# Performance work log

Hardware: AMD Instinct MI355X
Metric: run time of the kernel (lower is better)

The kernel has to match this reference:

```python
import jax, jax.numpy as jnp
import numpy as np

B, C1, C2, H, W = 16, 64, 64, 160, 160
K, KS, HID = 4, 3, 16  # K kernels, 3x3, hidden = max(int(64/16),16)=16
EPS = 1e-5


def setup_inputs() -> dict:
    key = jax.random.key(0)
    ks = jax.random.split(key, 8)
    fan_out = KS * KS * C2
    return {
        "x": jax.random.normal(ks[0], (B, C1, H, W), jnp.float32),
        # K candidate conv kernels and biases
        "Wk": jax.random.normal(ks[1], (K, C2, C1, KS, KS), jnp.float32) * np.sqrt(2.0 / fan_out),
        "bk": jnp.zeros((K, C2), jnp.float32),
        # attention trunk: 1x1 conv C1->HID (no bias), BN, ReLU
        "Wfc": jax.random.normal(ks[2], (HID, C1), jnp.float32) * 0.1,
        "gamma_h": jnp.ones((HID,), jnp.float32),
        "beta_h": jnp.zeros((HID,), jnp.float32),
        # four attention heads
        "Wf": jax.random.normal(ks[3], (C2, HID), jnp.float32) * 0.1,
        "bf": jnp.zeros((C2,), jnp.float32),
        "Ws": jax.random.normal(ks[4], (KS * KS, HID), jnp.float32) * 0.1,
        "bs": jnp.zeros((KS * KS,), jnp.float32),
        "Wc": jax.random.normal(ks[5], (C1, HID), jnp.float32) * 0.1,
        "bc": jnp.zeros((C1,), jnp.float32),
        "Ww": jax.random.normal(ks[6], (K, HID), jnp.float32) * 0.1,
        "bw": jnp.zeros((K,), jnp.float32),
        # outer BatchNorm2d params
        "gamma_o": jnp.ones((C2,), jnp.float32),
        "beta_o": jnp.zeros((C2,), jnp.float32),
    }


def reference(x, Wk, bk, Wfc, gamma_h, beta_h, Wf, bf, Ws, bs, Wc, bc, Ww, bw, gamma_o, beta_o):
    # ---- per-sample attention over K kernels ----
    ctx = x.mean(axis=(2, 3))                      # (B, C1)  global avg pool
    h = ctx @ Wfc.T                                # (B, HID) 1x1 conv == linear
    mu = h.mean(axis=0)
    var = h.var(axis=0)                            # biased, as torch BN training
    h = (h - mu) / jnp.sqrt(var + EPS) * gamma_h + beta_h
    h = jax.nn.relu(h)
    attn_f = jax.nn.sigmoid(h @ Wf.T + bf)         # (B, C2)
    attn_s = jax.nn.sigmoid(h @ Ws.T + bs).reshape(B, KS, KS)
    attn_c = jax.nn.sigmoid(h @ Wc.T + bc)         # (B, C1)
    attn_w = jax.nn.softmax(h @ Ww.T + bw, axis=-1)  # (B, K)

    # attn: (B, K, C2, C1, KS, KS) via broadcasting
    attn = (attn_w[:, :, None, None, None, None]
            * attn_f[:, None, :, None, None, None]
            * attn_c[:, None, None, :, None, None]
            * attn_s[:, None, None, None, :, :])
    weight = jnp.sum(attn * Wk[None], axis=1)      # (B, C2, C1, KS, KS)
    bias = attn_w @ bk                             # (B, C2)

    # ---- batched conv as grouped conv with groups=B ----
    out = jax.lax.conv_general_dilated(
        x.reshape(1, B * C1, H, W),
        weight.reshape(B * C2, C1, KS, KS),
        window_strides=(1, 1), padding=((1, 1), (1, 1)),
        dimension_numbers=('NCHW', 'OIHW', 'NCHW'),
        feature_group_count=B)                     # (1, B*C2, H, W)
    out = out.reshape(B, C2, H, W) + bias[:, :, None, None]

    # ---- outer BatchNorm2d (training stats) + SiLU ----
    mu_o = out.mean(axis=(0, 2, 3))
    var_o = out.var(axis=(0, 2, 3))
    out = (out - mu_o[None, :, None, None]) / jnp.sqrt(var_o + EPS)[None, :, None, None]
    out = out * gamma_o[None, :, None, None] + beta_o[None, :, None, None]
    return out * jax.nn.sigmoid(out)               # SiLU
```

## Files before the change

### kernel.cpp

```cpp
#include <hip/hip_runtime.h>
#include <math.h>

#define BB 16
#define C1 64
#define C2 64
#define HH 160
#define WW 160
#define KK 4
#define HID 16
#define EPS 1e-5f
#define HWSZ (HH*WW)
#define NPB (BB*HWSZ)

#define WS_AF    1024
#define WS_AC    2048
#define WS_AS    3072
#define WS_AW    3216
#define WS_BIAS  3280
#define WS_SC    4304
#define WS_SH    4368
#define WS_STATS 4432
#define NSLOT    32
#define WS_PART  8704
#define WS_WEFF  49664
#define WS_XBF   344576

typedef __attribute__((ext_vector_type(8)))  short bf16x8;
typedef __attribute__((ext_vector_type(16))) float f32x16;

__device__ __forceinline__ unsigned short f2bf(float f) {
    unsigned int u = __float_as_uint(f);
    unsigned int r = (u + 0x7FFFu + ((u >> 16) & 1u)) >> 16;
    return (unsigned short)r;
}

__device__ __forceinline__ void gload16(const void* g, void* l) {
    __builtin_amdgcn_global_load_lds(
        (const __attribute__((address_space(1))) unsigned int*)g,
        (__attribute__((address_space(3))) unsigned int*)l, 16, 0, 0);
}

__global__ __launch_bounds__(256) void xprep_kernel(const float* __restrict__ x,
                                                    float* __restrict__ ws) {
    __shared__ float lds[10240];
    int bcc = blockIdx.y;
    int rg = blockIdx.x;
    int t = threadIdx.x;

    const float* src = x + (size_t)bcc * 16 * HWSZ + (size_t)rg * 4 * WW;
    float4* l4 = (float4*)lds;
    #pragma unroll
    for (int i = 0; i < 10; ++i) {
        int g = i * 256 + t;
        int ch = g / 160, rem = g - ch * 160;
        l4[g] = *(const float4*)(src + (size_t)ch * HWSZ + rem * 4);
    }
    __syncthreads();

    {
        int ch = t >> 4, j = t & 15;
        float s = 0.f;
        #pragma unroll
        for (int m = 0; m < 40; ++m) s += lds[ch * 640 + j + 16 * m];
        #pragma unroll
        for (int o = 8; o > 0; o >>= 1) s += __shfl_down(s, o, 16);
        if (j == 0) ws[WS_PART + ((size_t)bcc * 40 + rg) * 16 + ch] = s;
    }

    uint4* dst = (uint4*)(ws + WS_XBF) + ((size_t)bcc * 160 + rg * 4) * 320;
    #pragma unroll
    for (int i = 0; i < 5; ++i) {
        int u = i * 256 + t;
        int row = u / 320, rem = u - row * 320;
        int col = rem >> 1, p = rem & 1;
        int h = p ^ ((col >> 2) & 1) ^ 1;
        union { uint4 q; unsigned short us[8]; } pk;
        #pragma unroll
        for (int k = 0; k < 8; ++k)
            pk.us[k] = f2bf(lds[(h * 8 + k) * 640 + row * 160 + col]);
        dst[u] = pk.q;
    }
}

__global__ void attn_kernel(float* __restrict__ ws,
    const float* __restrict__ Wfc, const float* __restrict__ gh, const float* __restrict__ bh,
    const float* __restrict__ Wf,  const float* __restrict__ bf,
    const float* __restrict__ Wsm, const float* __restrict__ bs,
    const float* __restrict__ Wc,  const float* __restrict__ bc,
    const float* __restrict__ Ww,  const float* __restrict__ bw,
    const float* __restrict__ bk) {
    __shared__ float ctxs[16][64];
    __shared__ float hs[16][16];
    __shared__ float aw[16][4];
    int t = threadIdx.x;

    #pragma unroll
    for (int q = 0; q < 4; ++q) {
        int idx = t * 4 + q;
        int b = idx >> 6, c1 = idx & 63;
        const float* pp = ws + WS_PART + ((size_t)(b * 4 + (c1 >> 4)) * 40) * 16 + (c1 & 15);
        float s = 0.f;
        #pragma unroll
        for (int rg = 0; rg < 40; ++rg) s += pp[rg * 16];
        ctxs[b][c1] = s * (1.0f / (float)HWSZ);
    }
    __syncthreads();
    {
        int b = t >> 4, j = t & 15;
        const float* wr = Wfc + j * 64;
        float s = 0.f;
        #pragma unroll
        for (int c = 0; c < 64; c++) s += ctxs[b][c] * wr[c];
        hs[b][j] = s;
    }
    __syncthreads();
    if (t < 16) {
        int j = t;
        float mu = 0.f;
        #pragma unroll
        for (int b = 0; b < 16; b++) mu += hs[b][j];
        mu *= (1.f / 16.f);
        float vr = 0.f;
        #pragma unroll
        for (int b = 0; b < 16; b++) { float d = hs[b][j] - mu; vr += d * d; }
        vr *= (1.f / 16.f);
        float sc = gh[j] * rsqrtf(vr + EPS);
        float sh = bh[j] - mu * sc;
        #pragma unroll
        for (int b = 0; b < 16; b++) {
            float v = hs[b][j] * sc + sh;
            hs[b][j] = v > 0.f ? v : 0.f;
        }
    }
    __syncthreads();
    if (t < 16) {
        int b = t;
        float l[4]; float mx = -1e30f;
        #pragma unroll
        for (int k = 0; k < 4; k++) {
            float s = bw[k];
            #pragma unroll
            for (int j = 0; j < 16; j++) s += hs[b][j] * Ww[k * 16 + j];
            l[k] = s; mx = fmaxf(mx, s);
        }
        float den = 0.f;
        #pragma unroll
        for (int k = 0; k < 4; k++) { l[k] = expf(l[k] - mx); den += l[k]; }
        float r = 1.f / den;
        #pragma unroll
        for (int k = 0; k < 4; k++) { float v = l[k] * r; aw[b][k] = v; ws[WS_AW + b * 4 + k] = v; }
    }
    #pragma unroll
    for (int q = 0; q < 4; q++) {
        int idx = t * 4 + q;
        int b = idx >> 6, c2 = idx & 63;
        float sf = bf[c2], sc2 = bc[c2];
        #pragma unroll
        for (int j = 0; j < 16; j++) {
            float hv = hs[b][j];
            sf  += hv * Wf[c2 * 16 + j];
            sc2 += hv * Wc[c2 * 16 + j];
        }
        ws[WS_AF + idx] = 1.f / (1.f + expf(-sf));
        ws[WS_AC + idx] = 1.f / (1.f + expf(-sc2));
    }
    if (t < 144) {
        int b = t / 9, uv = t % 9;
        float s = bs[uv];
        #pragma unroll
        for (int j = 0; j < 16; j++) s += hs[b][j] * Wsm[uv * 16 + j];
        ws[WS_AS + t] = 1.f / (1.f + expf(-s));
    }
    __syncthreads();
    #pragma unroll
    for (int q = 0; q < 4; q++) {
        int idx = t * 4 + q;
        int b = idx >> 6, c2 = idx & 63;
        float s = 0.f;
        #pragma unroll
        for (int k = 0; k < 4; k++) s += aw[b][k] * bk[k * 64 + c2];
        ws[WS_BIAS + idx] = s;
    }
    for (int i = t; i < NSLOT * 128; i += 256) ws[WS_STATS + i] = 0.f;
}

__global__ void wprep_kernel(const float* __restrict__ Wk, float* __restrict__ ws) {
    int b = blockIdx.y;
    int tid = blockIdx.x * 256 + threadIdx.x;
    int h = tid & 1;
    int c2 = (tid >> 1) & 63;
    int g = tid >> 7;
    int uv = g % 9;
    int chunk = g / 9;
    const float* awp = ws + WS_AW + b * 4;
    float aw0 = awp[0], aw1 = awp[1], aw2 = awp[2], aw3 = awp[3];
    float af = ws[WS_AF + b * 64 + c2];
    float as_ = ws[WS_AS + b * 9 + uv];
    union { uint4 q; unsigned short u[8]; } pk;
    #pragma unroll
    for (int j = 0; j < 8; ++j) {
        int c1 = chunk * 16 + h * 8 + j;
        const float* wp = Wk + (size_t)(c2 * 64 + c1) * 9 + uv;
        float s = aw0 * wp[0] + aw1 * wp[64 * 64 * 9] + aw2 * wp[2 * 64 * 64 * 9] + aw3 * wp[3 * 64 * 64 * 9];
        float w = s * af * ws[WS_AC + b * 64 + c1] * as_;
        pk.u[j] = f2bf(w);
    }
    int unit = ((chunk * 9 + uv) * 64 + c2) * 2 + (h ^ ((c2 >> 2) & 1));
    ((uint4*)(ws + WS_WEFF))[(size_t)b * 4608 + unit] = pk.q;
}

__launch_bounds__(256, 3)
__global__ void conv_kernel(const float* __restrict__ wsf, float* __restrict__ out) {
    __shared__ uint4 xs[4 * 162 * 2];
    __shared__ uint4 wsh[1152];
    __shared__ float bsh[64];
    __shared__ float sst[128];

    int id = blockIdx.x;
    int b = id & 15;
    int bx = id >> 4;
    int y0 = bx * 2;
    int t = threadIdx.x;
    int wv = t >> 6;
    int lane = t & 63;
    int l31 = lane & 31;
    int l5 = lane >> 5;
    int c2h = wv & 1;
    int rw = wv >> 1;

    if (t < 64) bsh[t] = wsf[WS_BIAS + b * 64 + t];
    if (t >= 64 && t < 192) sst[t - 64] = 0.f;
    if (t >= 192 && t < 208) {
        int q = t - 192;
        int r = q >> 2, side = (q >> 1) & 1, p = q & 1;
        xs[(r * 162 + side * 161) * 2 + p] = make_uint4(0, 0, 0, 0);
    }
    int rbad = (bx == 0) ? 0 : (bx == 79 ? 3 : -1);
    if (rbad >= 0) {
        for (int i = t; i < 320; i += 256)
            xs[(rbad * 162 + 1) * 2 + i] = make_uint4(0, 0, 0, 0);
    }

    const uint4* weff = (const uint4*)(wsf + WS_WEFF) + (size_t)b * 4608;
    const uint4* xbf  = (const uint4*)(wsf + WS_XBF);

    f32x16 acc[5];
    #pragma unroll
    for (int j = 0; j < 5; ++j)
        #pragma unroll
        for (int r = 0; r < 16; ++r) acc[j][r] = 0.f;

    int c2 = c2h * 32 + l31;
    int aswz = (l31 >> 2) & 1;
    for (int cc = 0; cc < 4; ++cc) {
        __syncthreads();
        for (int i = wv; i < 18; i += 4)
            gload16(weff + (size_t)cc * 1152 + i * 64 + lane, (char*)wsh + i * 1024);
        for (int i = wv; i < 20; i += 4) {
            int r = i / 5, seg = i % 5;
            int gy = y0 - 1 + r;
            if (gy >= 0 && gy < HH)
                gload16(xbf + (((size_t)b * 4 + cc) * 160 + gy) * 320 + seg * 64 + lane,
                        (char*)xs + ((r * 162 + 1) * 2 + seg * 64) * 16);
        }
        __syncthreads();

        #pragma unroll
        for (int uv = 0; uv < 9; ++uv) {
            bf16x8 a = *(bf16x8*)&wsh[(uv * 64 + c2) * 2 + (l5 ^ aswz)];
            int xr = rw + uv / 3;
            int v = uv % 3;
            #pragma unroll
            for (int j = 0; j < 5; ++j) {
                int col = j * 32 + l31 + v;
                bf16x8 bb = *(bf16x8*)&xs[(xr * 162 + col) * 2 + (l5 ^ (((col + 3) >> 2) & 1))];
                acc[j] = __builtin_amdgcn_mfma_f32_32x32x16_bf16(a, bb, acc[j], 0, 0, 0);
            }
        }
    }

    float* outb = out + (size_t)b * C2 * HWSZ + (size_t)(y0 + rw) * WW;
    int cb = c2h * 32 + 4 * l5;
    float sr[16], qr[16];
    #pragma unroll
    for (int r = 0; r < 16; ++r) {
        int c2r = cb + (r & 3) + 8 * (r >> 2);
        float bias = bsh[c2r];
        float s = 0.f, q = 0.f;
        #pragma unroll
        for (int j = 0; j < 5; ++j) {
            float v = acc[j][r] + bias;
            outb[(size_t)c2r * HWSZ + j * 32 + l31] = v;
            s += v;
            q = fmaf(v, v, q);
        }
        sr[r] = s; qr[r] = q;
    }
    #pragma unroll
    for (int k = 0; k < 4; ++k) {
        int m = 1 << k, n = 8 >> k;
        #pragma unroll
        for (int i = 0; i < 8; ++i) {
            if (i < n) {
                float ks = (l31 & m) ? sr[i + n] : sr[i];
                float ss = (l31 & m) ? sr[i] : sr[i + n];
                sr[i] = ks + __shfl_xor(ss, m, 64);
                float kq = (l31 & m) ? qr[i + n] : qr[i];
                float sq = (l31 & m) ? qr[i] : qr[i + n];
                qr[i] = kq + __shfl_xor(sq, m, 64);
            }
        }
    }
    sr[0] += __shfl_xor(sr[0], 16, 64);
    qr[0] += __shfl_xor(qr[0], 16, 64);
    if (l31 < 16) {
        int rf = ((l31 & 1) << 3) | ((l31 & 2) << 1) | ((l31 & 4) >> 1) | ((l31 & 8) >> 3);
        int c2r = cb + (rf & 3) + 8 * (rf >> 2);
        atomicAdd(&sst[c2r], sr[0]);
        atomicAdd(&sst[64 + c2r], qr[0]);
    }
    __syncthreads();
    if (t < 128) {
        int slot = id & (NSLOT - 1);
        atomicAdd((float*)wsf + WS_STATS + slot * 128 + t, sst[t]);
    }
}

__global__ void bnstat_kernel(float* __restrict__ ws, const float* __restrict__ go,
                              const float* __restrict__ bo) {
    int c = threadIdx.x;
    float s = 0.f, q = 0.f;
    for (int sl = 0; sl < NSLOT; sl++) {
        s += ws[WS_STATS + sl * 128 + c];
        q += ws[WS_STATS + sl * 128 + 64 + c];
    }
    float mu  = s * (1.0f / (float)NPB);
    float var = q * (1.0f / (float)NPB) - mu * mu;
    float sc  = go[c] * rsqrtf(var + EPS);
    ws[WS_SC + c] = sc;
    ws[WS_SH + c] = bo[c] - mu * sc;
}

__global__ void bnact_kernel(float* __restrict__ out, const float* __restrict__ ws) {
    __shared__ float sc[64], sh[64];
    if (threadIdx.x < 64) {
        sc[threadIdx.x] = ws[WS_SC + threadIdx.x];
        sh[threadIdx.x] = ws[WS_SH + threadIdx.x];
    }
    __syncthreads();
    const int n4 = BB * C2 * HWSZ / 4;
    for (int i = blockIdx.x * blockDim.x + threadIdx.x; i < n4; i += gridDim.x * blockDim.x) {
        float4 v = ((float4*)out)[i];
        int c = ((i * 4) / HWSZ) & 63;
        float s = sc[c], h = sh[c];
        v.x = v.x * s + h; v.y = v.y * s + h; v.z = v.z * s + h; v.w = v.w * s + h;
        v.x = v.x / (1.f + __expf(-v.x));
        v.y = v.y / (1.f + __expf(-v.y));
        v.z = v.z / (1.f + __expf(-v.z));
        v.w = v.w / (1.f + __expf(-v.w));
        ((float4*)out)[i] = v;
    }
}

extern "C" void kernel_launch(void* const* d_in, const int* in_sizes, int n_in,
                              void* d_out, int out_size, void* d_ws, size_t ws_size,
                              hipStream_t stream) {
    const float* x   = (const float*)d_in[0];
    const float* Wk  = (const float*)d_in[1];
    const float* bk  = (const float*)d_in[2];
    const float* Wfc = (const float*)d_in[3];
    const float* gh  = (const float*)d_in[4];
    const float* bh  = (const float*)d_in[5];
    const float* Wf  = (const float*)d_in[6];
    const float* bf  = (const float*)d_in[7];
    const float* Wsm = (const float*)d_in[8];
    const float* bs  = (const float*)d_in[9];
    const float* Wc  = (const float*)d_in[10];
    const float* bc  = (const float*)d_in[11];
    const float* Ww  = (const float*)d_in[12];
    const float* bw  = (const float*)d_in[13];
    const float* go  = (const float*)d_in[14];
    const float* bo  = (const float*)d_in[15];
    float* out = (float*)d_out;
    float* ws  = (float*)d_ws;

    xprep_kernel<<<dim3(40, 64), dim3(256), 0, stream>>>(x, ws);
    attn_kernel<<<dim3(1), dim3(256), 0, stream>>>(ws, Wfc, gh, bh, Wf, bf, Wsm, bs, Wc, bc, Ww, bw, bk);
    wprep_kernel<<<dim3(18, 16), dim3(256), 0, stream>>>(Wk, ws);
    conv_kernel<<<dim3(1280), dim3(256), 0, stream>>>(ws, out);
    bnstat_kernel<<<dim3(1), dim3(64), 0, stream>>>(ws, go, bo);
    bnact_kernel<<<dim3(2048), dim3(256), 0, stream>>>(out, ws);
}
```

Baseline: 131.4 us.

## Double-buffer conv LDS tiles to overlap next-chunk loads with MFMA compute

Shared-memory tiles for weights and input rows become two buffers, so the global-to-LDS loads for the next input-channel chunk are issued before computing the current one. Waits use explicit vmcnt counts and raw barriers in place of __syncthreads. Out-of-range halo rows are now loaded from a zeroed workspace region instead of being zeroed conditionally. This doubles LDS use and lowers the occupancy hint from 3 to 2 blocks per CU, trading latency hiding across waves for overlap inside each block.

```diff
diff --git a/kernel.cpp b/kernel.cpp
--- a/kernel.cpp
+++ b/kernel.cpp
@@ -22,8 +22,9 @@
 #define WS_STATS 4432
 #define NSLOT    32
 #define WS_PART  8704
-#define WS_WEFF  49664
-#define WS_XBF   344576
+#define WS_ZERO  49664
+#define WS_WEFF  50944
+#define WS_XBF   345856
 
 typedef __attribute__((ext_vector_type(8)))  short bf16x8;
 typedef __attribute__((ext_vector_type(16))) float f32x16;
@@ -182,6 +183,7 @@
         ws[WS_BIAS + idx] = s;
     }
     for (int i = t; i < NSLOT * 128; i += 256) ws[WS_STATS + i] = 0.f;
+    for (int i = t; i < 1280; i += 256) ws[WS_ZERO + i] = 0.f;
 }
 
 __global__ void wprep_kernel(const float* __restrict__ Wk, float* __restrict__ ws) {
@@ -209,10 +211,10 @@
     ((uint4*)(ws + WS_WEFF))[(size_t)b * 4608 + unit] = pk.q;
 }
 
-__launch_bounds__(256, 3)
+__launch_bounds__(256, 2)
 __global__ void conv_kernel(const float* __restrict__ wsf, float* __restrict__ out) {
-    __shared__ uint4 xs[4 * 162 * 2];
-    __shared__ uint4 wsh[1152];
+    __shared__ uint4 xs[2][4 * 162 * 2];
+    __shared__ uint4 wsh[2][1152];
     __shared__ float bsh[64];
     __shared__ float sst[128];
 
@@ -230,53 +232,63 @@
 
     if (t < 64) bsh[t] = wsf[WS_BIAS + b * 64 + t];
     if (t >= 64 && t < 192) sst[t - 64] = 0.f;
-    if (t >= 192 && t < 208) {
-        int q = t - 192;
+    if (t >= 192 && t < 224) {
+        int q = t - 192; int bq = q >> 4; q &= 15;
         int r = q >> 2, side = (q >> 1) & 1, p = q & 1;
-        xs[(r * 162 + side * 161) * 2 + p] = make_uint4(0, 0, 0, 0);
-    }
-    int rbad = (bx == 0) ? 0 : (bx == 79 ? 3 : -1);
-    if (rbad >= 0) {
-        for (int i = t; i < 320; i += 256)
-            xs[(rbad * 162 + 1) * 2 + i] = make_uint4(0, 0, 0, 0);
+        xs[bq][(r * 162 + side * 161) * 2 + p] = make_uint4(0, 0, 0, 0);
     }
 
     const uint4* weff = (const uint4*)(wsf + WS_WEFF) + (size_t)b * 4608;
     const uint4* xbf  = (const uint4*)(wsf + WS_XBF);
-
-    f32x16 acc[5];
-    #pragma unroll
-    for (int j = 0; j < 5; ++j)
-        #pragma unroll
-        for (int r = 0; r < 16; ++r) acc[j][r] = 0.f;
-
-    int c2 = c2h * 32 + l31;
-    int aswz = (l31 >> 2) & 1;
-    for (int cc = 0; cc < 4; ++cc) {
-        __syncthreads();
+    const uint4* zsrc = (const uint4*)(wsf + WS_ZERO);
+
+    auto stage = [&](int cc, int bq) {
         for (int i = wv; i < 18; i += 4)
-            gload16(weff + (size_t)cc * 1152 + i * 64 + lane, (char*)wsh + i * 1024);
+            gload16(weff + (size_t)cc * 1152 + i * 64 + lane, (char*)&wsh[bq][0] + i * 1024);
         for (int i = wv; i < 20; i += 4) {
             int r = i / 5, seg = i % 5;
             int gy = y0 - 1 + r;
-            if (gy >= 0 && gy < HH)
-                gload16(xbf + (((size_t)b * 4 + cc) * 160 + gy) * 320 + seg * 64 + lane,
-                        (char*)xs + ((r * 162 + 1) * 2 + seg * 64) * 16);
-        }
-        __syncthreads();
+            const uint4* src = (gy >= 0 && gy < HH)
+                ? xbf + (((size_t)b * 4 + cc) * 160 + gy) * 320 + seg * 64 + lane
+                : zsrc + seg * 64 + lane;
+            gload16(src, (char*)&xs[bq][0] + ((r * 162 + 1) * 2 + seg * 64) * 16);
+        }
+    };
+
+    f32x16 acc[5];
+    #pragma unroll
+    for (int j = 0; j < 5; ++j)
+        #pragma unroll
+        for (int r = 0; r < 16; ++r) acc[j][r] = 0.f;
+
+    stage(0, 0);
+
+    int c2 = c2h * 32 + l31;
+    int aswz = (l31 >> 2) & 1;
+    int cur = 0;
+    for (int cc = 0; cc < 4; ++cc) {
+        if (cc < 3) {
+            stage(cc + 1, cur ^ 1);
+            if (wv < 2) asm volatile("s_waitcnt vmcnt(10) lgkmcnt(0)\n\ts_barrier" ::: "memory");
+            else        asm volatile("s_waitcnt vmcnt(9) lgkmcnt(0)\n\ts_barrier" ::: "memory");
+        } else {
+            asm volatile("s_waitcnt vmcnt(0) lgkmcnt(0)\n\ts_barrier" ::: "memory");
+        }
 
         #pragma unroll
         for (int uv = 0; uv < 9; ++uv) {
-            bf16x8 a = *(bf16x8*)&wsh[(uv * 64 + c2) * 2 + (l5 ^ aswz)];
+            bf16x8 a = *(bf16x8*)&wsh[cur][(uv * 64 + c2) * 2 + (l5 ^ aswz)];
             int xr = rw + uv / 3;
             int v = uv % 3;
             #pragma unroll
             for (int j = 0; j < 5; ++j) {
                 int col = j * 32 + l31 + v;
-                bf16x8 bb = *(bf16x8*)&xs[(xr * 162 + col) * 2 + (l5 ^ (((col + 3) >> 2) & 1))];
+                bf16x8 bb = *(bf16x8*)&xs[cur][(xr * 162 + col) * 2 + (l5 ^ (((col + 3) >> 2) & 1))];
                 acc[j] = __builtin_amdgcn_mfma_f32_32x32x16_bf16(a, bb, acc[j], 0, 0, 0);
             }
         }
+        asm volatile("s_barrier" ::: "memory");
+        cur ^= 1;
     }
 
     float* outb = out + (size_t)b * C2 * HWSZ + (size_t)(y0 + rw) * WW;
```

Result: no change. 132.7 us (+1.0%).

## Load conv weights straight to registers, fuse BN stats into activation kernel

Applied to the files above, without the earlier changes.

The conv kernel stops staging the effective weights in shared memory. Each wave reads its nine A fragments directly from global memory into registers, and the bias is read from global memory instead of being cached in LDS. The stats epilogue is split into two groups of eight to lower register pressure, and launch bounds drop from 3 to 2 blocks per SM. The separate bnstat kernel is removed and its reduction runs redundantly in every bnact block, saving one launch at the cost of each of the 2048 blocks re-reading the 32 stat slots.

```diff
diff --git a/kernel.cpp b/kernel.cpp
--- a/kernel.cpp
+++ b/kernel.cpp
@@ -17,13 +17,11 @@
 #define WS_AS    3072
 #define WS_AW    3216
 #define WS_BIAS  3280
-#define WS_SC    4304
-#define WS_SH    4368
 #define WS_STATS 4432
 #define NSLOT    32
 #define WS_PART  8704
-#define WS_WEFF  49664
-#define WS_XBF   344576
+#define WS_WEFF  53760
+#define WS_XBF   348672
 
 typedef __attribute__((ext_vector_type(8)))  short bf16x8;
 typedef __attribute__((ext_vector_type(16))) float f32x16;
@@ -209,11 +207,9 @@
     ((uint4*)(ws + WS_WEFF))[(size_t)b * 4608 + unit] = pk.q;
 }
 
-__launch_bounds__(256, 3)
+__launch_bounds__(256, 2)
 __global__ void conv_kernel(const float* __restrict__ wsf, float* __restrict__ out) {
     __shared__ uint4 xs[4 * 162 * 2];
-    __shared__ uint4 wsh[1152];
-    __shared__ float bsh[64];
     __shared__ float sst[128];
 
     int id = blockIdx.x;
@@ -228,8 +224,7 @@
     int c2h = wv & 1;
     int rw = wv >> 1;
 
-    if (t < 64) bsh[t] = wsf[WS_BIAS + b * 64 + t];
-    if (t >= 64 && t < 192) sst[t - 64] = 0.f;
+    if (t < 128) sst[t] = 0.f;
     if (t >= 192 && t < 208) {
         int q = t - 192;
         int r = q >> 2, side = (q >> 1) & 1, p = q & 1;
@@ -241,83 +236,95 @@
             xs[(rbad * 162 + 1) * 2 + i] = make_uint4(0, 0, 0, 0);
     }
 
-    const uint4* weff = (const uint4*)(wsf + WS_WEFF) + (size_t)b * 4608;
+    const char* weffb = (const char*)(wsf + WS_WEFF) + (size_t)b * 73728;
     const uint4* xbf  = (const uint4*)(wsf + WS_XBF);
 
+    int c2 = c2h * 32 + l31;
+    int a_off = (c2 * 2 + (l5 ^ ((c2 >> 2) & 1))) * 16;
+
     f32x16 acc[5];
     #pragma unroll
     for (int j = 0; j < 5; ++j)
         #pragma unroll
         for (int r = 0; r < 16; ++r) acc[j][r] = 0.f;
 
-    int c2 = c2h * 32 + l31;
-    int aswz = (l31 >> 2) & 1;
     for (int cc = 0; cc < 4; ++cc) {
         __syncthreads();
-        for (int i = wv; i < 18; i += 4)
-            gload16(weff + (size_t)cc * 1152 + i * 64 + lane, (char*)wsh + i * 1024);
-        for (int i = wv; i < 20; i += 4) {
+        #pragma unroll
+        for (int k = 0; k < 5; ++k) {
+            int i = wv + 4 * k;
             int r = i / 5, seg = i % 5;
             int gy = y0 - 1 + r;
             if (gy >= 0 && gy < HH)
                 gload16(xbf + (((size_t)b * 4 + cc) * 160 + gy) * 320 + seg * 64 + lane,
                         (char*)xs + ((r * 162 + 1) * 2 + seg * 64) * 16);
         }
+        const char* wrow = weffb + cc * 18432;
+        bf16x8 av[9];
+        #pragma unroll
+        for (int uv = 0; uv < 9; ++uv)
+            av[uv] = *(const bf16x8*)(wrow + uv * 2048 + a_off);
         __syncthreads();
 
         #pragma unroll
         for (int uv = 0; uv < 9; ++uv) {
-            bf16x8 a = *(bf16x8*)&wsh[(uv * 64 + c2) * 2 + (l5 ^ aswz)];
             int xr = rw + uv / 3;
             int v = uv % 3;
             #pragma unroll
             for (int j = 0; j < 5; ++j) {
                 int col = j * 32 + l31 + v;
                 bf16x8 bb = *(bf16x8*)&xs[(xr * 162 + col) * 2 + (l5 ^ (((col + 3) >> 2) & 1))];
-                acc[j] = __builtin_amdgcn_mfma_f32_32x32x16_bf16(a, bb, acc[j], 0, 0, 0);
+                acc[j] = __builtin_amdgcn_mfma_f32_32x32x16_bf16(av[uv], bb, acc[j], 0, 0, 0);
             }
         }
     }
 
     float* outb = out + (size_t)b * C2 * HWSZ + (size_t)(y0 + rw) * WW;
     int cb = c2h * 32 + 4 * l5;
-    float sr[16], qr[16];
-    #pragma unroll
-    for (int r = 0; r < 16; ++r) {
-        int c2r = cb + (r & 3) + 8 * (r >> 2);
-        float bias = bsh[c2r];
-        float s = 0.f, q = 0.f;
-        #pragma unroll
-        for (int j = 0; j < 5; ++j) {
-            float v = acc[j][r] + bias;
-            outb[(size_t)c2r * HWSZ + j * 32 + l31] = v;
-            s += v;
-            q = fmaf(v, v, q);
-        }
-        sr[r] = s; qr[r] = q;
-    }
-    #pragma unroll
-    for (int k = 0; k < 4; ++k) {
-        int m = 1 << k, n = 8 >> k;
-        #pragma unroll
-        for (int i = 0; i < 8; ++i) {
-            if (i < n) {
-                float ks = (l31 & m) ? sr[i + n] : sr[i];
-                float ss = (l31 & m) ? sr[i] : sr[i + n];
-                sr[i] = ks + __shfl_xor(ss, m, 64);
-                float kq = (l31 & m) ? qr[i + n] : qr[i];
-                float sq = (l31 & m) ? qr[i] : qr[i + n];
-                qr[i] = kq + __shfl_xor(sq, m, 64);
+    #pragma unroll
+    for (int g = 0; g < 2; ++g) {
+        float sr[8], qr[8];
+        #pragma unroll
+        for (int m = 0; m < 8; ++m) {
+            int r = g * 8 + m;
+            int c2r = cb + (r & 3) + 8 * (r >> 2);
+            float bias = wsf[WS_BIAS + b * 64 + c2r];
+            float s = 0.f, q = 0.f;
+            #pragma unroll
+            for (int j = 0; j < 5; ++j) {
+                float v = acc[j][r] + bias;
+                outb[(size_t)c2r * HWSZ + j * 32 + l31] = v;
+                s += v;
+                q = fmaf(v, v, q);
             }
-        }
-    }
-    sr[0] += __shfl_xor(sr[0], 16, 64);
-    qr[0] += __shfl_xor(qr[0], 16, 64);
-    if (l31 < 16) {
-        int rf = ((l31 & 1) << 3) | ((l31 & 2) << 1) | ((l31 & 4) >> 1) | ((l31 & 8) >> 3);
-        int c2r = cb + (rf & 3) + 8 * (rf >> 2);
-        atomicAdd(&sst[c2r], sr[0]);
-        atomicAdd(&sst[64 + c2r], qr[0]);
+            sr[m] = s; qr[m] = q;
+        }
+        #pragma unroll
+        for (int k = 0; k < 3; ++k) {
+            int mm = 1 << k, n = 4 >> k;
+            #pragma unroll
+            for (int i = 0; i < 4; ++i) {
+                if (i < n) {
+                    float ks = (l31 & mm) ? sr[i + n] : sr[i];
+                    float ss = (l31 & mm) ? sr[i] : sr[i + n];
+                    sr[i] = ks + __shfl_xor(ss, mm, 64);
+                    float kq = (l31 & mm) ? qr[i + n] : qr[i];
+                    float sq = (l31 & mm) ? qr[i] : qr[i + n];
+                    qr[i] = kq + __shfl_xor(sq, mm, 64);
+                }
+            }
+        }
+        sr[0] += __shfl_xor(sr[0], 8, 64);
+        qr[0] += __shfl_xor(qr[0], 8, 64);
+        sr[0] += __shfl_xor(sr[0], 16, 64);
+        qr[0] += __shfl_xor(qr[0], 16, 64);
+        if (l31 < 8) {
+            int relem = ((l31 & 1) << 2) | (l31 & 2) | ((l31 & 4) >> 2);
+            int r = g * 8 + relem;
+            int c2r = cb + (r & 3) + 8 * (r >> 2);
+            atomicAdd(&sst[c2r], sr[0]);
+            atomicAdd(&sst[64 + c2r], qr[0]);
+        }
     }
     __syncthreads();
     if (t < 128) {
@@ -326,26 +333,22 @@
     }
 }
 
-__global__ void bnstat_kernel(float* __restrict__ ws, const float* __restrict__ go,
-                              const float* __restrict__ bo) {
-    int c = threadIdx.x;
-    float s = 0.f, q = 0.f;
-    for (int sl = 0; sl < NSLOT; sl++) {
-        s += ws[WS_STATS + sl * 128 + c];
-        q += ws[WS_STATS + sl * 128 + 64 + c];
-    }
-    float mu  = s * (1.0f / (float)NPB);
-    float var = q * (1.0f / (float)NPB) - mu * mu;
-    float sc  = go[c] * rsqrtf(var + EPS);
-    ws[WS_SC + c] = sc;
-    ws[WS_SH + c] = bo[c] - mu * sc;
-}
-
-__global__ void bnact_kernel(float* __restrict__ out, const float* __restrict__ ws) {
+__global__ void bnact_kernel(float* __restrict__ out, const float* __restrict__ ws,
+                             const float* __restrict__ go, const float* __restrict__ bo) {
     __shared__ float sc[64], sh[64];
     if (threadIdx.x < 64) {
-        sc[threadIdx.x] = ws[WS_SC + threadIdx.x];
-        sh[threadIdx.x] = ws[WS_SH + threadIdx.x];
+        int c = threadIdx.x;
+        float s = 0.f, q = 0.f;
+        #pragma unroll
+        for (int sl = 0; sl < NSLOT; sl++) {
+            s += ws[WS_STATS + sl * 128 + c];
+            q += ws[WS_STATS + sl * 128 + 64 + c];
+        }
+        float mu  = s * (1.0f / (float)NPB);
+        float var = q * (1.0f / (float)NPB) - mu * mu;
+        float scale = go[c] * rsqrtf(var + EPS);
+        sc[c] = scale;
+        sh[c] = bo[c] - mu * scale;
     }
     __syncthreads();
     const int n4 = BB * C2 * HWSZ / 4;
@@ -388,6 +391,5 @@
     attn_kernel<<<dim3(1), dim3(256), 0, stream>>>(ws, Wfc, gh, bh, Wf, bf, Wsm, bs, Wc, bc, Ww, bw, bk);
     wprep_kernel<<<dim3(18, 16), dim3(256), 0, stream>>>(Wk, ws);
     conv_kernel<<<dim3(1280), dim3(256), 0, stream>>>(ws, out);
-    bnstat_kernel<<<dim3(1), dim3(64), 0, stream>>>(ws, go, bo);
-    bnact_kernel<<<dim3(2048), dim3(256), 0, stream>>>(out, ws);
-}
+    bnact_kernel<<<dim3(2048), dim3(256), 0, stream>>>(out, ws, go, bo);
+}
```

Result: no change. 133.2 us (+1.4%).

## Store conv intermediate as bf16 in workspace and fold BN stats into activation kernel

Applied to the files above, without the earlier changes.

The conv kernel now writes its pre-normalization output as bf16 into a workspace buffer instead of fp32 into the output, which halves the intermediate write and the read in the BN/SiLU pass. The separate single-block bnstat kernel is removed, and every bnact block recomputes the per-channel scale and shift from the stat slots. This drops one launch and cuts memory traffic. In exchange it adds bf16 rounding error to the normalized output and needs a large workspace, with a fallback to the fp32 path when the workspace is too small.

```diff
diff --git a/kernel.cpp b/kernel.cpp
--- a/kernel.cpp
+++ b/kernel.cpp
@@ -17,13 +17,13 @@
 #define WS_AS    3072
 #define WS_AW    3216
 #define WS_BIAS  3280
-#define WS_SC    4304
-#define WS_SH    4368
 #define WS_STATS 4432
 #define NSLOT    32
 #define WS_PART  8704
-#define WS_WEFF  49664
-#define WS_XBF   344576
+#define WS_WEFF  53760
+#define WS_XBF   348672
+#define WS_OBF   13455872
+#define WS_NEED_BYTES 106252288ULL
 
 typedef __attribute__((ext_vector_type(8)))  short bf16x8;
 typedef __attribute__((ext_vector_type(16))) float f32x16;
@@ -209,6 +209,7 @@
     ((uint4*)(ws + WS_WEFF))[(size_t)b * 4608 + unit] = pk.q;
 }
 
+template<int OBF>
 __launch_bounds__(256, 3)
 __global__ void conv_kernel(const float* __restrict__ wsf, float* __restrict__ out) {
     __shared__ uint4 xs[4 * 162 * 2];
@@ -280,6 +281,8 @@
     }
 
     float* outb = out + (size_t)b * C2 * HWSZ + (size_t)(y0 + rw) * WW;
+    unsigned short* obfb = (unsigned short*)((float*)wsf + WS_OBF)
+                         + (size_t)b * C2 * HWSZ + (size_t)(y0 + rw) * WW;
     int cb = c2h * 32 + 4 * l5;
     float sr[16], qr[16];
     #pragma unroll
@@ -290,7 +293,8 @@
         #pragma unroll
         for (int j = 0; j < 5; ++j) {
             float v = acc[j][r] + bias;
-            outb[(size_t)c2r * HWSZ + j * 32 + l31] = v;
+            if (OBF) obfb[(size_t)c2r * HWSZ + j * 32 + l31] = f2bf(v);
+            else     outb[(size_t)c2r * HWSZ + j * 32 + l31] = v;
             s += v;
             q = fmaf(v, v, q);
         }
@@ -326,31 +330,38 @@
     }
 }
 
-__global__ void bnstat_kernel(float* __restrict__ ws, const float* __restrict__ go,
-                              const float* __restrict__ bo) {
-    int c = threadIdx.x;
-    float s = 0.f, q = 0.f;
-    for (int sl = 0; sl < NSLOT; sl++) {
-        s += ws[WS_STATS + sl * 128 + c];
-        q += ws[WS_STATS + sl * 128 + 64 + c];
-    }
-    float mu  = s * (1.0f / (float)NPB);
-    float var = q * (1.0f / (float)NPB) - mu * mu;
-    float sc  = go[c] * rsqrtf(var + EPS);
-    ws[WS_SC + c] = sc;
-    ws[WS_SH + c] = bo[c] - mu * sc;
-}
-
-__global__ void bnact_kernel(float* __restrict__ out, const float* __restrict__ ws) {
+template<int OBF>
+__global__ void bnact_kernel(float* __restrict__ out, const float* __restrict__ ws,
+                             const float* __restrict__ go, const float* __restrict__ bo) {
     __shared__ float sc[64], sh[64];
     if (threadIdx.x < 64) {
-        sc[threadIdx.x] = ws[WS_SC + threadIdx.x];
-        sh[threadIdx.x] = ws[WS_SH + threadIdx.x];
-    }
-    __syncthreads();
+        int c = threadIdx.x;
+        float s = 0.f, q = 0.f;
+        #pragma unroll
+        for (int sl = 0; sl < NSLOT; sl++) {
+            s += ws[WS_STATS + sl * 128 + c];
+            q += ws[WS_STATS + sl * 128 + 64 + c];
+        }
+        float mu  = s * (1.0f / (float)NPB);
+        float var = q * (1.0f / (float)NPB) - mu * mu;
+        float scale = go[c] * rsqrtf(var + EPS);
+        sc[c] = scale;
+        sh[c] = bo[c] - mu * scale;
+    }
+    __syncthreads();
+    const unsigned short* obf = (const unsigned short*)(ws + WS_OBF);
     const int n4 = BB * C2 * HWSZ / 4;
     for (int i = blockIdx.x * blockDim.x + threadIdx.x; i < n4; i += gridDim.x * blockDim.x) {
-        float4 v = ((float4*)out)[i];
+        float4 v;
+        if (OBF) {
+            ushort4 u = ((const ushort4*)obf)[i];
+            v.x = __uint_as_float((unsigned)u.x << 16);
+            v.y = __uint_as_float((unsigned)u.y << 16);
+            v.z = __uint_as_float((unsigned)u.z << 16);
+            v.w = __uint_as_float((unsigned)u.w << 16);
+        } else {
+            v = ((float4*)out)[i];
+        }
         int c = ((i * 4) / HWSZ) & 63;
         float s = sc[c], h = sh[c];
         v.x = v.x * s + h; v.y = v.y * s + h; v.z = v.z * s + h; v.w = v.w * s + h;
@@ -384,10 +395,16 @@
     float* out = (float*)d_out;
     float* ws  = (float*)d_ws;
 
+    bool use_obf = (ws_size >= WS_NEED_BYTES);
+
     xprep_kernel<<<dim3(40, 64), dim3(256), 0, stream>>>(x, ws);
     attn_kernel<<<dim3(1), dim3(256), 0, stream>>>(ws, Wfc, gh, bh, Wf, bf, Wsm, bs, Wc, bc, Ww, bw, bk);
     wprep_kernel<<<dim3(18, 16), dim3(256), 0, stream>>>(Wk, ws);
-    conv_kernel<<<dim3(1280), dim3(256), 0, stream>>>(ws, out);
-    bnstat_kernel<<<dim3(1), dim3(64), 0, stream>>>(ws, go, bo);
-    bnact_kernel<<<dim3(2048), dim3(256), 0, stream>>>(out, ws);
-}
+    if (use_obf) {
+        conv_kernel<1><<<dim3(1280), dim3(256), 0, stream>>>(ws, out);
+        bnact_kernel<1><<<dim3(2048), dim3(256), 0, stream>>>(out, ws, go, bo);
+    } else {
+        conv_kernel<0><<<dim3(1280), dim3(256), 0, stream>>>(ws, out);
+        bnact_kernel<0><<<dim3(2048), dim3(256), 0, stream>>>(out, ws, go, bo);
+    }
+}
```

Measured after the change: 129.8 us. Within noise of the previous version (-1.3%).
